# Kernel tuning notes

Hardware: AMD Instinct MI355X
Metric: run time of the kernel (lower is better)

## Reference

```python
import jax, jax.numpy as jnp
import numpy as np

T, DIM, H = 1024, 2048, 16
QLR, KVLR = 1024, 512
NOPE, ROPE, VD = 128, 64, 128
QKD = NOPE + ROPE          # 192
IH, ID, TOPK = 16, 128, 256
EPS = 1e-6

def rmsnorm(x, w):
    return x * jax.lax.rsqrt(jnp.mean(x * x, axis=-1, keepdims=True) + EPS) * w

def layernorm(x, w, b, eps=1e-5):
    m = jnp.mean(x, axis=-1, keepdims=True)
    v = jnp.mean((x - m) ** 2, axis=-1, keepdims=True)
    return (x - m) * jax.lax.rsqrt(v + eps) * w + b

def apply_rope(x, cos, sin):
    # non-interleaved: first half = real, second half = imag
    d = x.shape[-1] // 2
    while cos.ndim < x.ndim:
        cos, sin = cos[:, None], sin[:, None]
    x1, x2 = x[..., :d], x[..., d:]
    return jnp.concatenate([x1 * cos - x2 * sin, x1 * sin + x2 * cos], axis=-1)

def hadamard(x):
    # unnormalized Walsh-Hadamard on last dim (power of 2)
    n = x.shape[-1]
    shape = x.shape
    y, h = x, 1
    while h < n:
        y = y.reshape(shape[:-1] + (-1, 2 * h))
        a, b = y[..., :h], y[..., h:]
        y = jnp.concatenate([a + b, a - b], axis=-1)
        h *= 2
    return y.reshape(shape)

def rotate_activation(x):
    # half-swap then Hadamard on each half
    d = x.shape[-1] // 2
    x1, x2 = x[..., :d], x[..., d:]
    return jnp.concatenate([hadamard(x2), hadamard(x1)], axis=-1)

def setup_inputs() -> dict:
    key = jax.random.key(0)
    ks = jax.random.split(key, 10)
    s = 0.02
    w = lambda k, shp: jax.random.normal(k, shp, jnp.float32) * s
    pos = jnp.arange(T, dtype=jnp.float32)
    inv = 1.0 / (10000.0 ** (jnp.arange(0, ROPE, 2, dtype=jnp.float32) / ROPE))
    ang = pos[:, None] * inv[None, :]
    return {
        'hidden_states': jax.random.normal(ks[0], (T, DIM), jnp.float32),
        'rope_cos': jnp.cos(ang), 'rope_sin': jnp.sin(ang),
        'wq_a': w(ks[1], (QLR, DIM)),
        'q_norm_w': jnp.ones((QLR,), jnp.float32),
        'wq_b': w(ks[2], (H * QKD, QLR)),
        'wkv_a': w(ks[3], (KVLR + ROPE, DIM)),
        'kv_norm_w': jnp.ones((KVLR,), jnp.float32),
        'wkv_b': w(ks[4], (H * (NOPE + VD), KVLR)),
        'wo': w(ks[5], (DIM, H * VD)),
        'iq_norm_w': jnp.ones((QLR,), jnp.float32),
        'iwq_b': w(ks[6], (IH * ID, QLR)),
        'iwk': w(ks[7], (IH * ID, DIM)),
        'k_norm_w': jnp.ones((ID,), jnp.float32),
        'k_norm_b': jnp.zeros((ID,), jnp.float32),
        'wproj': w(ks[8], (IH, DIM)),
    }

def reference(hidden_states, rope_cos, rope_sin, wq_a, q_norm_w, wq_b,
              wkv_a, kv_norm_w, wkv_b, wo, iq_norm_w, iwq_b, iwk,
              k_norm_w, k_norm_b, wproj):
    x = hidden_states
    t = x.shape[0]
    qr = x @ wq_a.T                                   # [t, QLR]

    # ---- lightning indexer: top-k causal token selection ----
    iq = (rmsnorm(qr, iq_norm_w) @ iwq_b.T).reshape(t, IH, ID)
    iq = jnp.concatenate([apply_rope(iq[..., :ROPE], rope_cos, rope_sin), iq[..., ROPE:]], -1)
    iq = rotate_activation(iq)
    ik = layernorm((x @ iwk.T).reshape(t, IH, ID), k_norm_w, k_norm_b)
    ik = jnp.concatenate([apply_rope(ik[..., :ROPE], rope_cos, rope_sin), ik[..., ROPE:]], -1)
    ik = rotate_activation(ik)
    w = (x @ wproj.T) * (IH ** -0.5) * (ID ** -0.5)   # [t, IH]
    dots = jax.nn.relu(jnp.einsum('thd,shd->ths', iq, ik)) * w[:, :, None]
    score = dots.sum(axis=1)                          # [t, t]
    rows = jnp.arange(t)
    score = jnp.where(rows[None, :] <= rows[:, None], score, -jnp.inf)
    _, topk_idx = jax.lax.top_k(score, TOPK)          # [t, TOPK]
    valid = topk_idx <= rows[:, None]
    safe_idx = jnp.where(valid, topk_idx, 0)

    # ---- MLA latent projections ----
    q = (rmsnorm(qr, q_norm_w) @ wq_b.T).reshape(t, H, QKD)
    q_nope, q_pe = q[..., :NOPE], q[..., NOPE:]
    q_pe = apply_rope(q_pe, rope_cos, rope_sin)
    kv_a = x @ wkv_a.T                                # [t, KVLR+ROPE]
    kv = rmsnorm(kv_a[:, :KVLR], kv_norm_w)
    k_pe = apply_rope(kv_a[:, KVLR:], rope_cos, rope_sin)
    wkv = wkv_b.reshape(H, NOPE + VD, KVLR)
    w_k, w_v = wkv[:, :NOPE, :], wkv[:, NOPE:, :]
    q_nope_proj = jnp.einsum('thd,hdc->thc', q_nope, w_k)
    q_key = jnp.concatenate([q_nope_proj, q_pe], -1)  # [t, H, KVLR+ROPE]
    kv_key = jnp.concatenate([kv, k_pe], -1)          # [t, KVLR+ROPE]

    # ---- sparse attention over selected indices ----
    sel = kv_key[safe_idx]                            # [t, TOPK, KVLR+ROPE]
    scale = QKD ** -0.5
    logits = jnp.einsum('thc,tkc->thk', q_key, sel) * scale
    logits = jnp.where(valid[:, None, :], logits, -jnp.inf)
    attn = jax.nn.softmax(logits, axis=-1)
    out_latent = jnp.einsum('thk,tkc->thc', attn, sel[..., :KVLR])
    out_v = jnp.einsum('thc,hdc->thd', out_latent, w_v)
    return out_v.reshape(t, H * VD) @ wo.T            # [t, DIM]
```

## Files before the change

kernel.cpp:

```cpp
#include <hip/hip_runtime.h>
#include <hip/hip_bf16.h>
#include <math.h>

#define T_     1024
#define DIM_   2048
#define H_     16
#define QLR_   1024
#define KVLR_  512
#define NOPE_  128
#define ROPE_  64
#define VD_    128
#define QKD_   192
#define IH_    16
#define ID_    128
#define TOPK_  256
#define CKV_   576

#define SCALE_W    0.022097086912079608f
#define SCALE_LOG  0.07216878364870323f

typedef short bfrag __attribute__((ext_vector_type(8)));
typedef float ffrag __attribute__((ext_vector_type(4)));

__device__ __forceinline__ unsigned short f2bf(float f) {
    union { __hip_bfloat16 h; unsigned short u; } c; c.h = __float2bfloat16(f); return c.u;
}
__device__ __forceinline__ float bf2f(unsigned short u) {
    union { unsigned short u; __hip_bfloat16 h; } c; c.u = u; return __bfloat162float(c.h);
}

struct CastSeg { const float* src; unsigned short* hi; unsigned short* lo; };
struct CastDesc { CastSeg seg[6]; int bstart[7]; int nseg; };

__global__ __launch_bounds__(256) void castm_k(CastDesc d)
{
    int b = blockIdx.x, s = 0;
    #pragma unroll
    for (int i = 1; i < 6; ++i) if (i < d.nseg && b >= d.bstart[i]) s = i;
    long base = ((long)(b - d.bstart[s]) * 256 + threadIdx.x) * 4;
    float4 v = *(const float4*)(d.seg[s].src + base);
    ushort4 h4;
    h4.x = f2bf(v.x); h4.y = f2bf(v.y); h4.z = f2bf(v.z); h4.w = f2bf(v.w);
    *(ushort4*)(d.seg[s].hi + base) = h4;
    if (d.seg[s].lo) {
        ushort4 l4;
        l4.x = f2bf(v.x - bf2f(h4.x));
        l4.y = f2bf(v.y - bf2f(h4.y));
        l4.z = f2bf(v.z - bf2f(h4.z));
        l4.w = f2bf(v.w - bf2f(h4.w));
        *(ushort4*)(d.seg[s].lo + base) = l4;
    }
}

__global__ __launch_bounds__(256) void qrnorm_k(const float* __restrict__ qr,
    const float* __restrict__ iqw, const float* __restrict__ qw,
    unsigned short* __restrict__ qriq_hi, unsigned short* __restrict__ qriq_lo,
    unsigned short* __restrict__ qrq_hi)
{
    int t = blockIdx.x, tid = threadIdx.x;
    long base = (long)t * QLR_ + tid * 4;
    float4 v = *(const float4*)(qr + base);
    __shared__ float red[256];
    red[tid] = v.x * v.x + v.y * v.y + v.z * v.z + v.w * v.w;
    __syncthreads();
    for (int off = 128; off; off >>= 1) { if (tid < off) red[tid] += red[tid + off]; __syncthreads(); }
    float r = rsqrtf(red[0] / (float)QLR_ + 1e-6f);
    int col = tid * 4;
    float4 wi = *(const float4*)(iqw + col);
    float4 wq = *(const float4*)(qw + col);
    float s[4] = {v.x, v.y, v.z, v.w};
    float wiv[4] = {wi.x, wi.y, wi.z, wi.w};
    float wqv[4] = {wq.x, wq.y, wq.z, wq.w};
    ushort4 h4, l4, g4;
    unsigned short* hp = (unsigned short*)&h4;
    unsigned short* lp = (unsigned short*)&l4;
    unsigned short* gp = (unsigned short*)&g4;
    #pragma unroll
    for (int i = 0; i < 4; ++i) {
        float ai = s[i] * wiv[i] * r;
        float aq = s[i] * wqv[i] * r;
        hp[i] = f2bf(ai);
        lp[i] = f2bf(ai - bf2f(hp[i]));
        gp[i] = f2bf(aq);
    }
    *(ushort4*)(qriq_hi + base) = h4;
    *(ushort4*)(qriq_lo + base) = l4;
    *(ushort4*)(qrq_hi + base) = g4;
}

__global__ __launch_bounds__(256) void gemm_bt_mfma_k(
    const unsigned short* __restrict__ A, const unsigned short* __restrict__ B,
    void* __restrict__ Cv, long sA, long sB, long sC,
    int lda, int ldb, int ldc, int N, int K, int obf)
{
    A += (long)blockIdx.z * sA;
    B += (long)blockIdx.z * sB;
    __shared__ unsigned short As[128 * 40];
    __shared__ unsigned short Bs[128 * 40];
    const int tid = threadIdx.x;
    const int bm = blockIdx.y * 128, bn = blockIdx.x * 128;
    const int wave = tid >> 6, lane = tid & 63;
    const int wm = (wave >> 1) * 64, wn = (wave & 1) * 64;
    const int lm = lane & 15, quad = lane >> 4;

    ffrag acc[4][4];
    #pragma unroll
    for (int mi = 0; mi < 4; ++mi)
        #pragma unroll
        for (int ni = 0; ni < 4; ++ni)
            #pragma unroll
            for (int r = 0; r < 4; ++r) acc[mi][ni][r] = 0.f;

    const int srow = tid >> 1, shalf = tid & 1;
    const long aoff = (long)(bm + srow) * lda + shalf * 16;
    int brow = bn + srow; if (brow > N - 1) brow = N - 1;
    const long boff = (long)brow * ldb + shalf * 16;
    unsigned short* la = As + srow * 40 + shalf * 16;
    unsigned short* lb = Bs + srow * 40 + shalf * 16;

    uint4 va0 = *(const uint4*)(A + aoff);
    uint4 va1 = *(const uint4*)(A + aoff + 8);
    uint4 vb0 = *(const uint4*)(B + boff);
    uint4 vb1 = *(const uint4*)(B + boff + 8);

    for (int k0 = 0; k0 < K; k0 += 32) {
        __syncthreads();
        *(uint4*)la = va0; *(uint4*)(la + 8) = va1;
        *(uint4*)lb = vb0; *(uint4*)(lb + 8) = vb1;
        __syncthreads();
        if (k0 + 32 < K) {
            va0 = *(const uint4*)(A + aoff + k0 + 32);
            va1 = *(const uint4*)(A + aoff + k0 + 40);
            vb0 = *(const uint4*)(B + boff + k0 + 32);
            vb1 = *(const uint4*)(B + boff + k0 + 40);
        }
        bfrag af[4], bf[4];
        #pragma unroll
        for (int mi = 0; mi < 4; ++mi)
            af[mi] = *(const bfrag*)(As + (wm + mi * 16 + lm) * 40 + quad * 8);
        #pragma unroll
        for (int ni = 0; ni < 4; ++ni)
            bf[ni] = *(const bfrag*)(Bs + (wn + ni * 16 + lm) * 40 + quad * 8);
        #pragma unroll
        for (int mi = 0; mi < 4; ++mi)
            #pragma unroll
            for (int ni = 0; ni < 4; ++ni)
                acc[mi][ni] = __builtin_amdgcn_mfma_f32_16x16x32_bf16(
                    af[mi], bf[ni], acc[mi][ni], 0, 0, 0);
    }

    #pragma unroll
    for (int mi = 0; mi < 4; ++mi)
        #pragma unroll
        for (int ni = 0; ni < 4; ++ni) {
            int n = bn + wn + ni * 16 + lm;
            if (n < N) {
                int mb = bm + wm + mi * 16 + quad * 4;
                if (obf) {
                    unsigned short* C = (unsigned short*)Cv + (long)blockIdx.z * sC;
                    #pragma unroll
                    for (int r = 0; r < 4; ++r)
                        C[(long)(mb + r) * ldc + n] = f2bf(acc[mi][ni][r]);
                } else {
                    float* C = (float*)Cv + (long)blockIdx.z * sC;
                    #pragma unroll
                    for (int r = 0; r < 4; ++r)
                        C[(long)(mb + r) * ldc + n] = acc[mi][ni][r];
                }
            }
        }
}

struct GSeg {
    const void* A; const void* Al; const void* B; const void* Bl;
    void* C; void* C2;
    long sA, sB, sC;
    int lda, ldb, ldc, N, K, bnx, bmx, mode, obf;
};
struct GDesc { GSeg seg[4]; int bstart[5]; int nseg; };

__global__ __launch_bounds__(256) void mgemm_k(GDesc d)
{
    __shared__ unsigned short Ahs[64 * 72], Als[64 * 72], Bhs[64 * 72], Bls[64 * 72];
    const int tid = threadIdx.x;
    const int b = blockIdx.x;
    int s = 0;
    #pragma unroll
    for (int i = 1; i < 4; ++i) if (i < d.nseg && b >= d.bstart[i]) s = i;
    const int rel = b - d.bstart[s];
    const int mode = d.seg[s].mode;

    if (mode == 2) {
        const float* src = (const float*)d.seg[s].A;
        unsigned short* hi = (unsigned short*)d.seg[s].C;
        unsigned short* lo = (unsigned short*)d.seg[s].C2;
        long base = ((long)rel * 256 + tid) * 4;
        float4 v = *(const float4*)(src + base);
        ushort4 h4;
        h4.x = f2bf(v.x); h4.y = f2bf(v.y); h4.z = f2bf(v.z); h4.w = f2bf(v.w);
        *(ushort4*)(hi + base) = h4;
        if (lo) {
            ushort4 l4;
            l4.x = f2bf(v.x - bf2f(h4.x));
            l4.y = f2bf(v.y - bf2f(h4.y));
            l4.z = f2bf(v.z - bf2f(h4.z));
            l4.w = f2bf(v.w - bf2f(h4.w));
            *(ushort4*)(lo + base) = l4;
        }
        return;
    }
    if (mode == 3) {
        const float* x = (const float*)d.seg[s].A;
        const float* wproj = (const float*)d.seg[s].B;
        float* wt = (float*)d.seg[s].C;
        float* xs = (float*)Ahs;
        int t = rel;
        for (int c = tid; c < DIM_; c += 256) xs[c] = x[(long)t * DIM_ + c];
        __syncthreads();
        int wave = tid >> 6, lane = tid & 63;
        #pragma unroll
        for (int i = 0; i < 4; ++i) {
            int h = wave * 4 + i;
            float sum = 0.f;
            for (int c = lane; c < DIM_; c += 64) sum += xs[c] * wproj[(long)h * DIM_ + c];
            for (int off = 32; off; off >>= 1) sum += __shfl_xor(sum, off, 64);
            if (lane == 0) wt[(long)t * IH_ + h] = sum * SCALE_W;
        }
        return;
    }
    if (mode == 4) {
        const float* in = (const float*)d.seg[s].A;
        unsigned short* out = (unsigned short*)d.seg[s].C;
        int h = rel >> 6, c0 = (rel & 15) * 32, d0 = ((rel >> 4) & 3) * 32;
        float (*tt)[33] = (float(*)[33])(void*)Ahs;
        int tx = tid & 31, ty = tid >> 5;
        #pragma unroll
        for (int i = 0; i < 4; ++i)
            tt[ty + i * 8][tx] = in[(long)(h * 256 + d0 + ty + i * 8) * 512 + c0 + tx];
        __syncthreads();
        #pragma unroll
        for (int i = 0; i < 4; ++i)
            out[((long)h * 512 + c0 + ty + i * 8) * 128 + d0 + tx] = f2bf(tt[tx][ty + i * 8]);
        return;
    }
    if (mode == 5) {
        const float* q = (const float*)d.seg[s].A;
        const float* cosb = (const float*)d.seg[s].B;
        const float* sinb = (const float*)d.seg[s].Bl;
        unsigned short* qk = (unsigned short*)d.seg[s].C;
        int row = rel * 8 + (tid >> 5);
        int i = tid & 31;
        int t = row / H_;
        const float* qp = q + (long)row * QKD_ + NOPE_;
        float x1 = qp[i], x2 = qp[i + 32];
        float c = cosb[t * 32 + i], sn = sinb[t * 32 + i];
        unsigned short* o = qk + (long)row * CKV_ + 512;
        o[i]      = f2bf(x1 * c - x2 * sn);
        o[i + 32] = f2bf(x1 * sn + x2 * c);
        return;
    }

    const GSeg g = d.seg[s];
    const bool three = (mode == 1);
    const int per = g.bnx * g.bmx;
    const int z = rel / per;
    const int r2 = rel - z * per;
    const int bm = (r2 / g.bnx) * 64, bn = (r2 % g.bnx) * 64;
    const unsigned short* A  = (const unsigned short*)g.A + (long)z * g.sA;
    const unsigned short* B  = (const unsigned short*)g.B + (long)z * g.sB;
    const unsigned short* Alp = (const unsigned short*)g.Al;
    const unsigned short* Blp = (const unsigned short*)g.Bl;

    const int wave = tid >> 6, lane = tid & 63;
    const int wm = (wave >> 1) * 32, wn = (wave & 1) * 32;
    const int lm = lane & 15, quad = lane >> 4;

    ffrag acc[2][2];
    #pragma unroll
    for (int mi = 0; mi < 2; ++mi)
        #pragma unroll
        for (int ni = 0; ni < 2; ++ni)
            #pragma unroll
            for (int r = 0; r < 4; ++r) acc[mi][ni][r] = 0.f;

    const int srow = tid >> 2, schunk = tid & 3;
    const long aoff = (long)(bm + srow) * g.lda + schunk * 8;
    int brow = bn + srow; if (brow > g.N - 1) brow = g.N - 1;
    const long boff = (long)brow * g.ldb + schunk * 8;
    const int loff = srow * 72 + schunk * 8;

    uint4 va0, va1, vb0, vb1, wa0, wa1, wb0, wb1;
    va0 = *(const uint4*)(A + aoff);
    va1 = *(const uint4*)(A + aoff + 32);
    vb0 = *(const uint4*)(B + boff);
    vb1 = *(const uint4*)(B + boff + 32);
    if (three) {
        wa0 = *(const uint4*)(Alp + aoff);
        wa1 = *(const uint4*)(Alp + aoff + 32);
        wb0 = *(const uint4*)(Blp + boff);
        wb1 = *(const uint4*)(Blp + boff + 32);
    }

    for (int k0 = 0; k0 < g.K; k0 += 64) {
        __syncthreads();
        *(uint4*)(Ahs + loff) = va0; *(uint4*)(Ahs + loff + 32) = va1;
        *(uint4*)(Bhs + loff) = vb0; *(uint4*)(Bhs + loff + 32) = vb1;
        if (three) {
            *(uint4*)(Als + loff) = wa0; *(uint4*)(Als + loff + 32) = wa1;
            *(uint4*)(Bls + loff) = wb0; *(uint4*)(Bls + loff + 32) = wb1;
        }
        __syncthreads();
        if (k0 + 64 < g.K) {
            va0 = *(const uint4*)(A + aoff + k0 + 64);
            va1 = *(const uint4*)(A + aoff + k0 + 96);
            vb0 = *(const uint4*)(B + boff + k0 + 64);
            vb1 = *(const uint4*)(B + boff + k0 + 96);
            if (three) {
                wa0 = *(const uint4*)(Alp + aoff + k0 + 64);
                wa1 = *(const uint4*)(Alp + aoff + k0 + 96);
                wb0 = *(const uint4*)(Blp + boff + k0 + 64);
                wb1 = *(const uint4*)(Blp + boff + k0 + 96);
            }
        }
        bfrag ah[2][2], bh[2][2], al[2][2], bl[2][2];
        #pragma unroll
        for (int mi = 0; mi < 2; ++mi)
            #pragma unroll
            for (int ks = 0; ks < 2; ++ks)
                ah[mi][ks] = *(const bfrag*)(Ahs + (wm + mi * 16 + lm) * 72 + ks * 32 + quad * 8);
        #pragma unroll
        for (int ni = 0; ni < 2; ++ni)
            #pragma unroll
            for (int ks = 0; ks < 2; ++ks)
                bh[ni][ks] = *(const bfrag*)(Bhs + (wn + ni * 16 + lm) * 72 + ks * 32 + quad * 8);
        if (three) {
            #pragma unroll
            for (int mi = 0; mi < 2; ++mi)
                #pragma unroll
                for (int ks = 0; ks < 2; ++ks)
                    al[mi][ks] = *(const bfrag*)(Als + (wm + mi * 16 + lm) * 72 + ks * 32 + quad * 8);
            #pragma unroll
            for (int ni = 0; ni < 2; ++ni)
                #pragma unroll
                for (int ks = 0; ks < 2; ++ks)
                    bl[ni][ks] = *(const bfrag*)(Bls + (wn + ni * 16 + lm) * 72 + ks * 32 + quad * 8);
        }
        #pragma unroll
        for (int mi = 0; mi < 2; ++mi)
            #pragma unroll
            for (int ni = 0; ni < 2; ++ni) {
                acc[mi][ni] = __builtin_amdgcn_mfma_f32_16x16x32_bf16(ah[mi][0], bh[ni][0], acc[mi][ni], 0, 0, 0);
                if (three) {
                    acc[mi][ni] = __builtin_amdgcn_mfma_f32_16x16x32_bf16(ah[mi][0], bl[ni][0], acc[mi][ni], 0, 0, 0);
                    acc[mi][ni] = __builtin_amdgcn_mfma_f32_16x16x32_bf16(al[mi][0], bh[ni][0], acc[mi][ni], 0, 0, 0);
                }
                acc[mi][ni] = __builtin_amdgcn_mfma_f32_16x16x32_bf16(ah[mi][1], bh[ni][1], acc[mi][ni], 0, 0, 0);
                if (three) {
                    acc[mi][ni] = __builtin_amdgcn_mfma_f32_16x16x32_bf16(ah[mi][1], bl[ni][1], acc[mi][ni], 0, 0, 0);
                    acc[mi][ni] = __builtin_amdgcn_mfma_f32_16x16x32_bf16(al[mi][1], bh[ni][1], acc[mi][ni], 0, 0, 0);
                }
            }
    }

    #pragma unroll
    for (int mi = 0; mi < 2; ++mi)
        #pragma unroll
        for (int ni = 0; ni < 2; ++ni) {
            int n = bn + wn + ni * 16 + lm;
            if (n < g.N) {
                int mb = bm + wm + mi * 16 + quad * 4;
                if (g.obf) {
                    unsigned short* C = (unsigned short*)g.C + (long)z * g.sC;
                    #pragma unroll
                    for (int r = 0; r < 4; ++r)
                        C[(long)(mb + r) * g.ldc + n] = f2bf(acc[mi][ni][r]);
                } else {
                    float* C = (float*)g.C + (long)z * g.sC;
                    #pragma unroll
                    for (int r = 0; r < 4; ++r)
                        C[(long)(mb + r) * g.ldc + n] = acc[mi][ni][r];
                }
            }
        }
}

__global__ __launch_bounds__(256) void mtrans_k(
    const float* __restrict__ iq, unsigned short* __restrict__ iqh, unsigned short* __restrict__ iql,
    const float* __restrict__ ik, unsigned short* __restrict__ ikh, unsigned short* __restrict__ ikl,
    const float* __restrict__ knw, const float* __restrict__ knb,
    const float* __restrict__ kva, unsigned short* __restrict__ kvb, const float* __restrict__ kvnw,
    const float* __restrict__ cosb, const float* __restrict__ sinb)
{
    __shared__ float red[256];
    __shared__ float rsh;
    const int b = blockIdx.x, tid = threadIdx.x;
    if (b < 8192) {
        const bool isq = b < 4096;
        int rb = isq ? b : b - 4096;
        int row = rb * 4 + (tid >> 6);
        int p = tid & 63;
        int t = row >> 4;
        const float* src = isq ? iq : ik;
        float a = src[(long)row * 128 + p];
        float bb = src[(long)row * 128 + 64 + p];
        if (!isq) {
            float ssum = a + bb;
            #pragma unroll
            for (int o = 1; o < 64; o <<= 1) ssum += __shfl_xor(ssum, o, 64);
            float m = ssum * (1.f / 128.f);
            float da = a - m, db = bb - m;
            float v = da * da + db * db;
            #pragma unroll
            for (int o = 1; o < 64; o <<= 1) v += __shfl_xor(v, o, 64);
            float r = rsqrtf(v * (1.f / 128.f) + 1e-5f);
            a = da * r * knw[p] + knb[p];
            bb = db * r * knw[64 + p] + knb[64 + p];
        }
        float c = cosb[t * 32 + (p & 31)], sn = sinb[t * 32 + (p & 31)];
        float asw = __shfl_xor(a, 32, 64);
        a = (p < 32) ? (a * c - asw * sn) : (asw * sn + a * c);
        #pragma unroll
        for (int h = 1; h < 64; h <<= 1) {
            float a2 = __shfl_xor(a, h, 64);
            float b2 = __shfl_xor(bb, h, 64);
            a = (p & h) ? (a2 - a) : (a + a2);
            bb = (p & h) ? (b2 - bb) : (bb + b2);
        }
        unsigned short* hi = isq ? iqh : ikh;
        unsigned short* lo = isq ? iql : ikl;
        unsigned short hb = f2bf(bb), ha = f2bf(a);
        hi[(long)row * 128 + p] = hb;
        hi[(long)row * 128 + 64 + p] = ha;
        lo[(long)row * 128 + p] = f2bf(bb - bf2f(hb));
        lo[(long)row * 128 + 64 + p] = f2bf(a - bf2f(ha));
    } else {
        int t = b - 8192;
        const float* a = kva + (long)t * CKV_;
        unsigned short* o = kvb + (long)t * CKV_;
        float v0 = a[tid], v1 = a[tid + 256];
        red[tid] = v0 * v0 + v1 * v1; __syncthreads();
        for (int off = 128; off; off >>= 1) { if (tid < off) red[tid] += red[tid + off]; __syncthreads(); }
        if (tid == 0) rsh = rsqrtf(red[0] / (float)KVLR_ + 1e-6f);
        __syncthreads();
        float rs = rsh;
        o[tid]       = f2bf(v0 * rs * kvnw[tid]);
        o[tid + 256] = f2bf(v1 * rs * kvnw[tid + 256]);
        if (tid < 32) {
            float x1 = a[512 + tid], x2 = a[544 + tid];
            float c = cosb[t * 32 + tid], sn = sinb[t * 32 + tid];
            o[512 + tid] = f2bf(x1 * c - x2 * sn);
            o[544 + tid] = f2bf(x1 * sn + x2 * c);
        }
    }
}

__global__ __launch_bounds__(256) void score3_k(
    const unsigned short* __restrict__ iqh, const unsigned short* __restrict__ iql,
    const unsigned short* __restrict__ ikh, const unsigned short* __restrict__ ikl,
    const float* __restrict__ wtok, float* __restrict__ scorep)
{
    const int bt = blockIdx.y, bs = blockIdx.x;
    if (bs > bt) return;
    const int hz = blockIdx.z;
    const int h0 = hz * 4;
    float* score = scorep + (long)hz * (T_ * T_);
    __shared__ unsigned short Ah[64 * 72], Al[64 * 72], Bh[64 * 72], Bl[64 * 72];
    __shared__ float wts[64][16];
    const int tid = threadIdx.x;
    const int wave = tid >> 6, lane = tid & 63;
    const int wm = (wave >> 1) * 32, wn = (wave & 1) * 32;
    const int lm = lane & 15, quad = lane >> 4;
    const int t0 = bt * 64, s0 = bs * 64;
    const int srow = tid >> 2, schunk = tid & 3;
    const int loff = srow * 72 + schunk * 8;

    for (int e = tid; e < 1024; e += 256)
        wts[e >> 4][e & 15] = wtok[(long)(t0 + (e >> 4)) * IH_ + (e & 15)];

    const long abase = (long)(t0 + srow) * 2048 + schunk * 8 + h0 * 128;
    const long bbase = (long)(s0 + srow) * 2048 + schunk * 8 + h0 * 128;

    uint4 pah0 = *(const uint4*)(iqh + abase);
    uint4 pah1 = *(const uint4*)(iqh + abase + 32);
    uint4 pal0 = *(const uint4*)(iql + abase);
    uint4 pal1 = *(const uint4*)(iql + abase + 32);
    uint4 pbh0 = *(const uint4*)(ikh + bbase);
    uint4 pbh1 = *(const uint4*)(ikh + bbase + 32);
    uint4 pbl0 = *(const uint4*)(ikl + bbase);
    uint4 pbl1 = *(const uint4*)(ikl + bbase + 32);

    float accf[2][2][4] = {};

    for (int hh = 0; hh < 4; ++hh) {
        const int h = h0 + hh;
        ffrag acch[2][2];
        #pragma unroll
        for (int mi = 0; mi < 2; ++mi)
            #pragma unroll
            for (int ni = 0; ni < 2; ++ni)
                #pragma unroll
                for (int r = 0; r < 4; ++r) acch[mi][ni][r] = 0.f;

        #pragma unroll
        for (int k0 = 0; k0 < ID_; k0 += 64) {
            __syncthreads();
            *(uint4*)(Ah + loff) = pah0; *(uint4*)(Ah + loff + 32) = pah1;
            *(uint4*)(Al + loff) = pal0; *(uint4*)(Al + loff + 32) = pal1;
            *(uint4*)(Bh + loff) = pbh0; *(uint4*)(Bh + loff + 32) = pbh1;
            *(uint4*)(Bl + loff) = pbl0; *(uint4*)(Bl + loff + 32) = pbl1;
            __syncthreads();
            int step = hh * 2 + (k0 >> 6) + 1;
            if (step < 8) {
                long off = (long)(step >> 1) * 128 + (step & 1) * 64;
                pah0 = *(const uint4*)(iqh + abase + off);
                pah1 = *(const uint4*)(iqh + abase + off + 32);
                pal0 = *(const uint4*)(iql + abase + off);
                pal1 = *(const uint4*)(iql + abase + off + 32);
                pbh0 = *(const uint4*)(ikh + bbase + off);
                pbh1 = *(const uint4*)(ikh + bbase + off + 32);
                pbl0 = *(const uint4*)(ikl + bbase + off);
                pbl1 = *(const uint4*)(ikl + bbase + off + 32);
            }
            bfrag ahf[2][2], alf[2][2], bhf[2][2], blf[2][2];
            #pragma unroll
            for (int mi = 0; mi < 2; ++mi)
                #pragma unroll
                for (int ks = 0; ks < 2; ++ks) {
                    ahf[mi][ks] = *(const bfrag*)(Ah + (wm + mi * 16 + lm) * 72 + ks * 32 + quad * 8);
                    alf[mi][ks] = *(const bfrag*)(Al + (wm + mi * 16 + lm) * 72 + ks * 32 + quad * 8);
                }
            #pragma unroll
            for (int ni = 0; ni < 2; ++ni)
                #pragma unroll
                for (int ks = 0; ks < 2; ++ks) {
                    bhf[ni][ks] = *(const bfrag*)(Bh + (wn + ni * 16 + lm) * 72 + ks * 32 + quad * 8);
                    blf[ni][ks] = *(const bfrag*)(Bl + (wn + ni * 16 + lm) * 72 + ks * 32 + quad * 8);
                }
            #pragma unroll
            for (int mi = 0; mi < 2; ++mi)
                #pragma unroll
                for (int ni = 0; ni < 2; ++ni) {
                    acch[mi][ni] = __builtin_amdgcn_mfma_f32_16x16x32_bf16(ahf[mi][0], bhf[ni][0], acch[mi][ni], 0, 0, 0);
                    acch[mi][ni] = __builtin_amdgcn_mfma_f32_16x16x32_bf16(ahf[mi][0], blf[ni][0], acch[mi][ni], 0, 0, 0);
                    acch[mi][ni] = __builtin_amdgcn_mfma_f32_16x16x32_bf16(alf[mi][0], bhf[ni][0], acch[mi][ni], 0, 0, 0);
                    acch[mi][ni] = __builtin_amdgcn_mfma_f32_16x16x32_bf16(ahf[mi][1], bhf[ni][1], acch[mi][ni], 0, 0, 0);
                    acch[mi][ni] = __builtin_amdgcn_mfma_f32_16x16x32_bf16(ahf[mi][1], blf[ni][1], acch[mi][ni], 0, 0, 0);
                    acch[mi][ni] = __builtin_amdgcn_mfma_f32_16x16x32_bf16(alf[mi][1], bhf[ni][1], acch[mi][ni], 0, 0, 0);
                }
        }
        #pragma unroll
        for (int mi = 0; mi < 2; ++mi) {
            float wr[4];
            #pragma unroll
            for (int r = 0; r < 4; ++r) wr[r] = wts[wm + mi * 16 + quad * 4 + r][h];
            #pragma unroll
            for (int ni = 0; ni < 2; ++ni)
                #pragma unroll
                for (int r = 0; r < 4; ++r)
                    accf[mi][ni][r] += fmaxf(acch[mi][ni][r], 0.f) * wr[r];
        }
    }
    #pragma unroll
    for (int mi = 0; mi < 2; ++mi)
        #pragma unroll
        for (int ni = 0; ni < 2; ++ni) {
            int s = s0 + wn + ni * 16 + lm;
            int tb = t0 + wm + mi * 16 + quad * 4;
            #pragma unroll
            for (int r = 0; r < 4; ++r)
                score[(long)(tb + r) * T_ + s] = accf[mi][ni][r];
        }
}

__global__ __launch_bounds__(512) void topk_k(const float* __restrict__ scorep, int* __restrict__ topk)
{
    int t = blockIdx.x, tid = threadIdx.x;
    __shared__ float v[1024];
    __shared__ int ix[1024];
    const float* p0 = scorep + (long)t * T_;
    const float* p1 = p0 + (long)1 * T_ * T_;
    const float* p2 = p0 + (long)2 * T_ * T_;
    const float* p3 = p0 + (long)3 * T_ * T_;
    for (int i = tid; i < 1024; i += 512) {
        v[i] = (i <= t) ? (p0[i] + p1[i] + p2[i] + p3[i]) : -INFINITY;
        ix[i] = i;
    }
    __syncthreads();
    for (int k = 2; k <= 1024; k <<= 1) {
        for (int j = k >> 1; j > 0; j >>= 1) {
            for (int i = tid; i < 1024; i += 512) {
                int l = i ^ j;
                if (l > i) {
                    bool up = ((i & k) == 0);
                    float vi = v[i], vl = v[l];
                    int xi = ix[i], xl = ix[l];
                    bool iBetter = (vi > vl) || (vi == vl && xi < xl);
                    bool doSwap = up ? !iBetter : iBetter;
                    if (doSwap) { v[i] = vl; v[l] = vi; ix[i] = xl; ix[l] = xi; }
                }
            }
            __syncthreads();
        }
    }
    if (tid < 256) topk[(long)t * TOPK_ + tid] = ix[tid];
}

__global__ __launch_bounds__(256, 4) void attn3_k(
    const unsigned short* __restrict__ qkeyb, const unsigned short* __restrict__ kvb,
    const int* __restrict__ topkp, unsigned short* __restrict__ olat)
{
    __shared__ __align__(16) unsigned short U[13568];
    __shared__ float red[16 * 17];
    __shared__ int kidx[256];
    unsigned short* Qbf = U;
    float*          Lg  = (float*)U;
    unsigned short* VT0 = U;
    unsigned short* VT1 = U + 4608;
    unsigned short* Pbf = U + 9344;

    const int t = blockIdx.x, tid = threadIdx.x;
    const int wave = tid >> 6, lane = tid & 63;
    const int lm = lane & 15, quad = lane >> 4;

    kidx[tid] = topkp[(long)t * TOPK_ + tid];
    const uint2* q2 = (const uint2*)(qkeyb + (long)t * (H_ * CKV_));
    #pragma unroll
    for (int rep = 0; rep < 9; ++rep) {
        int e = rep * 256 + tid;
        uint2 v = q2[e];
        int f = e * 4, h = f / CKV_, c = f - h * CKV_;
        *(uint2*)(Qbf + h * 584 + c) = v;
    }
    int myk0 = topkp[(long)t * TOPK_ + wave * 64 + 0 * 16 + lm];
    int myk1 = topkp[(long)t * TOPK_ + wave * 64 + 1 * 16 + lm];
    int myk2 = topkp[(long)t * TOPK_ + wave * 64 + 2 * 16 + lm];
    int myk3 = topkp[(long)t * TOPK_ + wave * 64 + 3 * 16 + lm];
    __syncthreads();

    ffrag acc[4];
    #pragma unroll
    for (int ni = 0; ni < 4; ++ni)
        #pragma unroll
        for (int r = 0; r < 4; ++r) acc[ni][r] = 0.f;

    const unsigned short* kb0 = kvb + (long)myk0 * CKV_ + quad * 8;
    const unsigned short* kb1 = kvb + (long)myk1 * CKV_ + quad * 8;
    const unsigned short* kb2 = kvb + (long)myk2 * CKV_ + quad * 8;
    const unsigned short* kb3 = kvb + (long)myk3 * CKV_ + quad * 8;

    bfrag ba[4], bb[4], bc[4];
    #define LDT(DST, C) { \
        DST[0] = *(const bfrag*)(kb0 + (C)); \
        DST[1] = *(const bfrag*)(kb1 + (C)); \
        DST[2] = *(const bfrag*)(kb2 + (C)); \
        DST[3] = *(const bfrag*)(kb3 + (C)); }
    #define PHA_STEP(I, BUF) { \
        bfrag af = *(const bfrag*)(Qbf + lm * 584 + (I) * 32 + quad * 8); \
        _Pragma("unroll") \
        for (int ni = 0; ni < 4; ++ni) \
            acc[ni] = __builtin_amdgcn_mfma_f32_16x16x32_bf16(af, BUF[ni], acc[ni], 0, 0, 0); \
        if ((I) < 15) LDT(BUF, (I) * 32 + 96) }

    LDT(ba, 0) LDT(bb, 32) LDT(bc, 64)
    PHA_STEP(0, ba)  PHA_STEP(1, bb)  PHA_STEP(2, bc)
    PHA_STEP(3, ba)  PHA_STEP(4, bb)  PHA_STEP(5, bc)
    PHA_STEP(6, ba)  PHA_STEP(7, bb)  PHA_STEP(8, bc)
    PHA_STEP(9, ba)  PHA_STEP(10, bb) PHA_STEP(11, bc)
    PHA_STEP(12, ba) PHA_STEP(13, bb) PHA_STEP(14, bc)
    PHA_STEP(15, ba) PHA_STEP(16, bb) PHA_STEP(17, bc)
    #undef PHA_STEP
    #undef LDT

    __syncthreads();
    #pragma unroll
    for (int ni = 0; ni < 4; ++ni)
        #pragma unroll
        for (int r = 0; r < 4; ++r)
            Lg[(quad * 4 + r) * 260 + wave * 64 + ni * 16 + lm] = acc[ni][r];
    __syncthreads();

    {
        int h = tid >> 4, j = tid & 15;
        float m = -INFINITY;
        #pragma unroll
        for (int kk = 0; kk < 16; ++kk) {
            int key = j * 16 + kk;
            if (kidx[key] <= t) m = fmaxf(m, Lg[h * 260 + key]);
        }
        red[h * 17 + j] = m;
        __syncthreads();
        float mh = -INFINITY;
        #pragma unroll
        for (int jj = 0; jj < 16; ++jj) mh = fmaxf(mh, red[h * 17 + jj]);
        __syncthreads();
        float s = 0.f;
        float pv[16];
        #pragma unroll
        for (int kk = 0; kk < 16; ++kk) {
            int key = j * 16 + kk;
            float e = (kidx[key] <= t) ? expf(Lg[h * 260 + key] * SCALE_LOG - mh * SCALE_LOG) : 0.f;
            pv[kk] = e; s += e;
        }
        red[h * 17 + j] = s;
        __syncthreads();
        float sh = 0.f;
        #pragma unroll
        for (int jj = 0; jj < 16; ++jj) sh += red[h * 17 + jj];
        float inv = 1.f / sh;
        #pragma unroll
        for (int kk = 0; kk < 16; ++kk)
            Pbf[h * 264 + j * 16 + kk] = f2bf(pv[kk] * inv);
    }

    const int kpair = tid & 15, cgrp = tid >> 4;
    ffrag acc2[2];
    #pragma unroll
    for (int ci = 0; ci < 2; ++ci)
        #pragma unroll
        for (int r = 0; r < 4; ++r) acc2[ci][r] = 0.f;

    uint4 ga0, gb0, ga1, gb1;
    #define PREFB(GA, GB, IT) { \
        int ka_ = kidx[((IT) & 7) * 32 + 2 * kpair]; \
        int kb_ = kidx[((IT) & 7) * 32 + 2 * kpair + 1]; \
        long co_ = (long)(((IT) >> 3) * 128 + cgrp * 8); \
        GA = *(const uint4*)(kvb + (long)ka_ * CKV_ + co_); \
        GB = *(const uint4*)(kvb + (long)kb_ * CKV_ + co_); }
    #define STOREB(GA, GB, BUF) { \
        const unsigned short* pa_ = (const unsigned short*)&GA; \
        const unsigned short* pb_ = (const unsigned short*)&GB; \
        _Pragma("unroll") \
        for (int i_ = 0; i_ < 8; ++i_) \
            *(unsigned int*)((BUF) + (cgrp * 8 + i_) * 36 + 2 * kpair) = \
                (unsigned int)pa_[i_] | ((unsigned int)pb_[i_] << 16); }
    #define MFMAB(BUF, IT) { \
        bfrag pa = *(const bfrag*)(Pbf + lm * 264 + ((IT) & 7) * 32 + quad * 8); \
        _Pragma("unroll") \
        for (int ci = 0; ci < 2; ++ci) { \
            int c = wave * 32 + ci * 16 + lm; \
            bfrag bv; \
            ((uint2*)&bv)[0] = *(const uint2*)((BUF) + c * 36 + quad * 8); \
            ((uint2*)&bv)[1] = *(const uint2*)((BUF) + c * 36 + quad * 8 + 4); \
            acc2[ci] = __builtin_amdgcn_mfma_f32_16x16x32_bf16(pa, bv, acc2[ci], 0, 0, 0); } }
    #define OLATST(IT) { \
        int p_ = (IT) >> 3; \
        _Pragma("unroll") \
        for (int ci = 0; ci < 2; ++ci) \
            _Pragma("unroll") \
            for (int r = 0; r < 4; ++r) \
                olat[((long)t * H_ + quad * 4 + r) * 512 + p_ * 128 + wave * 32 + ci * 16 + lm] \
                    = f2bf(acc2[ci][r]); \
        _Pragma("unroll") \
        for (int ci = 0; ci < 2; ++ci) \
            _Pragma("unroll") \
            for (int r = 0; r < 4; ++r) acc2[ci][r] = 0.f; }
    #define LGKBAR() { asm volatile("s_waitcnt lgkmcnt(0)" ::: "memory"); \
                       __builtin_amdgcn_s_barrier(); }

    PREFB(ga0, gb0, 0);
    PREFB(ga1, gb1, 1);
    LGKBAR();
    STOREB(ga0, gb0, VT0);
    LGKBAR();
    for (int it = 0; it < 32; it += 2) {
        STOREB(ga1, gb1, VT1);
        MFMAB(VT0, it);
        if (it + 2 < 32) PREFB(ga0, gb0, it + 2);
        LGKBAR();
        if (it + 2 < 32) STOREB(ga0, gb0, VT0);
        MFMAB(VT1, it + 1);
        if (it + 3 < 32) PREFB(ga1, gb1, it + 3);
        if (((it + 1) & 7) == 7) OLATST(it + 1);
        LGKBAR();
    }
    #undef PREFB
    #undef STOREB
    #undef MFMAB
    #undef OLATST
    #undef LGKBAR
}

extern "C" void kernel_launch(void* const* d_in, const int* in_sizes, int n_in,
                              void* d_out, int out_size, void* d_ws, size_t ws_size,
                              hipStream_t stream)
{
    const float* x          = (const float*)d_in[0];
    const float* cosb       = (const float*)d_in[1];
    const float* sinb       = (const float*)d_in[2];
    const float* wq_a       = (const float*)d_in[3];
    const float* q_norm_w   = (const float*)d_in[4];
    const float* wq_b       = (const float*)d_in[5];
    const float* wkv_a      = (const float*)d_in[6];
    const float* kv_norm_w  = (const float*)d_in[7];
    const float* wkv_b      = (const float*)d_in[8];
    const float* wo         = (const float*)d_in[9];
    const float* iq_norm_w  = (const float*)d_in[10];
    const float* iwq_b      = (const float*)d_in[11];
    const float* iwk        = (const float*)d_in[12];
    const float* k_norm_w   = (const float*)d_in[13];
    const float* k_norm_b   = (const float*)d_in[14];
    const float* wproj      = (const float*)d_in[15];
    float* out = (float*)d_out;

    float* ws    = (float*)d_ws;
    float* qr    = ws;
    float* wtok  = ws + 1049600;
    int*   topk  = (int*)(ws + 1655808);
    float* qkey  = ws + 1917952;
    float* outv  = ws + 11355136;
    float* U0    = ws + 13452288;
    float* iq    = U0;
    float* ik    = U0 + 2097152;
    float* kva   = U0 + 4194304;
    float* qbuf  = U0 + 4784128;
    float* scorep = U0;

    unsigned short* qkey_u = (unsigned short*)qkey;
    unsigned short* wqa_hi  = qkey_u;
    unsigned short* wqa_lo  = qkey_u + 2097152;
    unsigned short* iwk_hi  = qkey_u + 4194304;
    unsigned short* iwk_lo  = qkey_u + 8388608;
    unsigned short* iwqb_hi = qkey_u + 12582912;
    unsigned short* iwqb_lo = qkey_u + 14680064;
    unsigned short* qriq_hi = qkey_u + 16777216;
    unsigned short* qriq_lo = qkey_u + 17825792;
    unsigned short* iqbf_hi = qkey_u;
    unsigned short* iqbf_lo = qkey_u + 2097152;
    unsigned short* ikbf_hi = qkey_u + 4194304;
    unsigned short* ikbf_lo = qkey_u + 6291456;
    unsigned short* qkey_bf = qkey_u;
    unsigned short* wkvb_bf = qkey_u + 9437184;
    unsigned short* wo_bf   = qkey_u;
    unsigned short* q_u     = (unsigned short*)qbuf;
    unsigned short* x_hi    = q_u;
    unsigned short* x_lo    = q_u + 2097152;
    unsigned short* wkva_hi = q_u + 4194304;
    unsigned short* outv_u  = (unsigned short*)outv;
    unsigned short* wqb_hi  = outv_u;
    unsigned short* qrq_hi  = outv_u + 3145728;
    unsigned short* outv_bf = outv_u;
    unsigned short* qbf     = (unsigned short*)iq;
    unsigned short* wkT     = (unsigned short*)ik;
    unsigned short* kvb     = (unsigned short*)qr;
    unsigned short* olat_bf = (unsigned short*)U0;

    {
        CastDesc d;
        d.seg[0] = { x,      x_hi,    x_lo    };
        d.seg[1] = { wq_a,   wqa_hi,  wqa_lo  };
        d.seg[2] = { iwk,    iwk_hi,  iwk_lo  };
        d.seg[3] = { iwq_b,  iwqb_hi, iwqb_lo };
        d.seg[4] = { wkv_a,  wkva_hi, nullptr };
        d.seg[5] = { wq_b,   wqb_hi,  nullptr };
        d.bstart[0] = 0;     d.bstart[1] = 2048;  d.bstart[2] = 4096;
        d.bstart[3] = 8192;  d.bstart[4] = 10240; d.bstart[5] = 11392;
        d.bstart[6] = 14464; d.nseg = 6;
        castm_k<<<14464, 256, 0, stream>>>(d);
    }

    {
        GDesc d{};
        d.nseg = 3;
        d.bstart[0] = 0; d.bstart[1] = 256; d.bstart[2] = 768; d.bstart[3] = 1792;
        GSeg& s0 = d.seg[0];
        s0.A = x_hi; s0.Al = x_lo; s0.B = wqa_hi; s0.Bl = wqa_lo; s0.C = qr;
        s0.lda = DIM_; s0.ldb = DIM_; s0.ldc = QLR_; s0.N = QLR_; s0.K = DIM_;
        s0.bnx = 16; s0.bmx = 16; s0.mode = 1; s0.obf = 0;
        GSeg& s1 = d.seg[1];
        s1.A = x_hi; s1.Al = x_lo; s1.B = iwk_hi; s1.Bl = iwk_lo; s1.C = ik;
        s1.lda = DIM_; s1.ldb = DIM_; s1.ldc = IH_ * ID_; s1.N = IH_ * ID_; s1.K = DIM_;
        s1.bnx = 32; s1.bmx = 16; s1.mode = 1; s1.obf = 0;
        GSeg& s2 = d.seg[2];
        s2.A = x; s2.B = wproj; s2.C = wtok; s2.mode = 3;
        mgemm_k<<<1792, 256, 0, stream>>>(d);
    }

    qrnorm_k<<<T_, 256, 0, stream>>>(qr, iq_norm_w, q_norm_w, qriq_hi, qriq_lo, qrq_hi);

    {
        GDesc d{};
        d.nseg = 3;
        d.bstart[0] = 0; d.bstart[1] = 512; d.bstart[2] = 656; d.bstart[3] = 2704;
        GSeg& s0 = d.seg[0];
        s0.A = qriq_hi; s0.Al = qriq_lo; s0.B = iwqb_hi; s0.Bl = iwqb_lo; s0.C = iq;
        s0.lda = QLR_; s0.ldb = QLR_; s0.ldc = IH_ * ID_; s0.N = IH_ * ID_; s0.K = QLR_;
        s0.bnx = 32; s0.bmx = 16; s0.mode = 1; s0.obf = 0;
        GSeg& s1 = d.seg[1];
        s1.A = x_hi; s1.B = wkva_hi; s1.C = kva;
        s1.lda = DIM_; s1.ldb = DIM_; s1.ldc = CKV_; s1.N = CKV_; s1.K = DIM_;
        s1.bnx = 9; s1.bmx = 16; s1.mode = 0; s1.obf = 0;
        GSeg& s2 = d.seg[2];
        s2.A = wkv_b; s2.C = wkvb_bf; s2.C2 = nullptr; s2.mode = 2;
        mgemm_k<<<2704, 256, 0, stream>>>(d);
    }

    {
        GDesc d{};
        d.nseg = 1;
        d.bstart[0] = 0; d.bstart[1] = 768;
        GSeg& s0 = d.seg[0];
        s0.A = qrq_hi; s0.B = wqb_hi; s0.C = qbuf;
        s0.lda = QLR_; s0.ldb = QLR_; s0.ldc = H_ * QKD_; s0.N = H_ * QKD_; s0.K = QLR_;
        s0.bnx = 48; s0.bmx = 16; s0.mode = 0; s0.obf = 0;
        mgemm_k<<<768, 256, 0, stream>>>(d);
    }

    mtrans_k<<<9216, 256, 0, stream>>>(iq, iqbf_hi, iqbf_lo, ik, ikbf_hi, ikbf_lo,
                                       k_norm_w, k_norm_b, kva, kvb, kv_norm_w, cosb, sinb);

    score3_k<<<dim3(T_/64, T_/64, 4), 256, 0, stream>>>(iqbf_hi, iqbf_lo, ikbf_hi, ikbf_lo, wtok, scorep);
    topk_k<<<T_, 512, 0, stream>>>(scorep, topk);

    {
        GDesc d{};
        d.nseg = 3;
        d.bstart[0] = 0; d.bstart[1] = 3072; d.bstart[2] = 4096; d.bstart[3] = 6144;
        GSeg& s0 = d.seg[0];
        s0.A = qbuf; s0.C = qbf; s0.C2 = nullptr; s0.mode = 2;
        GSeg& s1 = d.seg[1];
        s1.A = wkv_b; s1.C = wkT; s1.mode = 4;
        GSeg& s2 = d.seg[2];
        s2.A = qbuf; s2.B = cosb; s2.Bl = sinb; s2.C = qkey_bf; s2.mode = 5;
        mgemm_k<<<6144, 256, 0, stream>>>(d);
    }

    gemm_bt_mfma_k<<<dim3(KVLR_/128, T_/128, H_), 256, 0, stream>>>(
        qbf, wkT, qkey_bf, 192L, 65536L, 576L, H_*QKD_, ID_, H_*CKV_, KVLR_, ID_, 1);

    attn3_k<<<T_, 256, 0, stream>>>(qkey_bf, kvb, topk, olat_bf);

    {
        GDesc d{};
        d.nseg = 2;
        d.bstart[0] = 0; d.bstart[1] = 512; d.bstart[2] = 4608;
        GSeg& s0 = d.seg[0];
        s0.A = olat_bf; s0.B = wkvb_bf + (long)NOPE_ * KVLR_; s0.C = outv_bf;
        s0.sA = 512; s0.sB = (long)(NOPE_ + VD_) * KVLR_; s0.sC = VD_;
        s0.lda = H_ * KVLR_; s0.ldb = KVLR_; s0.ldc = H_ * VD_; s0.N = VD_; s0.K = KVLR_;
        s0.bnx = 2; s0.bmx = 16; s0.mode = 0; s0.obf = 1;
        GSeg& s1 = d.seg[1];
        s1.A = wo; s1.C = wo_bf; s1.C2 = nullptr; s1.mode = 2;
        mgemm_k<<<4608, 256, 0, stream>>>(d);
    }

    {
        GDesc d{};
        d.nseg = 1;
        d.bstart[0] = 0; d.bstart[1] = 512;
        GSeg& s0 = d.seg[0];
        s0.A = outv_bf; s0.B = wo_bf; s0.C = out;
        s0.lda = H_ * VD_; s0.ldb = H_ * VD_; s0.ldc = DIM_; s0.N = DIM_; s0.K = H_ * VD_;
        s0.bnx = 32; s0.bmx = 16; s0.mode = 0; s0.obf = 0;
        mgemm_k<<<512, 256, 0, stream>>>(d);
    }

    (void)in_sizes; (void)n_in; (void)out_size; (void)ws_size;
}
```

Before: 493.4 us.

## Merge transform kernel into wq_b GEMM launch and move wo cast into attention

Folds the separate indexer-transform and kv-norm kernel into the wq_b GEMM launch as new segment modes 6 and 7. The standalone wo bf16 cast moves from the output-projection launch into extra blocks of the attention kernel, and two scratch buffers swap locations to allow this. The aim is fewer kernel launches and letting independent small work fill idle compute units next to the GEMM and attention. In exchange, the fused kernels carry more code and shared memory, which could lower occupancy. Co-scheduling also now depends on the buffers not aliasing.

Result: no change. 500.5 us (+1.4%).

```diff
diff --git a/kernel.cpp b/kernel.cpp
--- a/kernel.cpp
+++ b/kernel.cpp
@@ -259,6 +259,75 @@
         o[i + 32] = f2bf(x1 * sn + x2 * c);
         return;
     }
+    if (mode == 6) {
+        const float* src = (const float*)d.seg[s].A;
+        unsigned short* hi = (unsigned short*)d.seg[s].C;
+        unsigned short* lo = (unsigned short*)d.seg[s].C2;
+        const float* cosb = (const float*)d.seg[s].B;
+        const float* sinb = (const float*)d.seg[s].Bl;
+        const float* knw  = (const float*)d.seg[s].Al;
+        const float* knb  = (const float*)(void*)d.seg[s].sA;
+        int row = rel * 4 + (tid >> 6);
+        int p = tid & 63;
+        int t = row >> 4;
+        float a = src[(long)row * 128 + p];
+        float bb = src[(long)row * 128 + 64 + p];
+        if (knw) {
+            float ssum = a + bb;
+            #pragma unroll
+            for (int o = 1; o < 64; o <<= 1) ssum += __shfl_xor(ssum, o, 64);
+            float m = ssum * (1.f / 128.f);
+            float da = a - m, db = bb - m;
+            float v = da * da + db * db;
+            #pragma unroll
+            for (int o = 1; o < 64; o <<= 1) v += __shfl_xor(v, o, 64);
+            float r = rsqrtf(v * (1.f / 128.f) + 1e-5f);
+            a = da * r * knw[p] + knb[p];
+            bb = db * r * knw[64 + p] + knb[64 + p];
+        }
+        float c = cosb[t * 32 + (p & 31)], sn = sinb[t * 32 + (p & 31)];
+        float asw = __shfl_xor(a, 32, 64);
+        a = (p < 32) ? (a * c - asw * sn) : (asw * sn + a * c);
+        #pragma unroll
+        for (int h = 1; h < 64; h <<= 1) {
+            float a2 = __shfl_xor(a, h, 64);
+            float b2 = __shfl_xor(bb, h, 64);
+            a = (p & h) ? (a2 - a) : (a + a2);
+            bb = (p & h) ? (b2 - bb) : (bb + b2);
+        }
+        unsigned short hb = f2bf(bb), ha = f2bf(a);
+        hi[(long)row * 128 + p] = hb;
+        hi[(long)row * 128 + 64 + p] = ha;
+        lo[(long)row * 128 + p] = f2bf(bb - bf2f(hb));
+        lo[(long)row * 128 + 64 + p] = f2bf(a - bf2f(ha));
+        return;
+    }
+    if (mode == 7) {
+        const float* kva = (const float*)d.seg[s].A;
+        unsigned short* kvb = (unsigned short*)d.seg[s].C;
+        const float* kvnw = (const float*)d.seg[s].B;
+        const float* cosb = (const float*)d.seg[s].Bl;
+        const float* sinb = (const float*)d.seg[s].Al;
+        float* red = (float*)Ahs;
+        int t = rel;
+        const float* a = kva + (long)t * CKV_;
+        unsigned short* o = kvb + (long)t * CKV_;
+        float v0 = a[tid], v1 = a[tid + 256];
+        red[tid] = v0 * v0 + v1 * v1; __syncthreads();
+        for (int off = 128; off; off >>= 1) { if (tid < off) red[tid] += red[tid + off]; __syncthreads(); }
+        if (tid == 0) red[256] = rsqrtf(red[0] / (float)KVLR_ + 1e-6f);
+        __syncthreads();
+        float rs = red[256];
+        o[tid]       = f2bf(v0 * rs * kvnw[tid]);
+        o[tid + 256] = f2bf(v1 * rs * kvnw[tid + 256]);
+        if (tid < 32) {
+            float x1 = a[512 + tid], x2 = a[544 + tid];
+            float c = cosb[t * 32 + tid], sn = sinb[t * 32 + tid];
+            o[512 + tid] = f2bf(x1 * c - x2 * sn);
+            o[544 + tid] = f2bf(x1 * sn + x2 * c);
+        }
+        return;
+    }
 
     const GSeg g = d.seg[s];
     const bool three = (mode == 1);
@@ -382,76 +451,6 @@
                 }
             }
         }
-}
-
-__global__ __launch_bounds__(256) void mtrans_k(
-    const float* __restrict__ iq, unsigned short* __restrict__ iqh, unsigned short* __restrict__ iql,
-    const float* __restrict__ ik, unsigned short* __restrict__ ikh, unsigned short* __restrict__ ikl,
-    const float* __restrict__ knw, const float* __restrict__ knb,
-    const float* __restrict__ kva, unsigned short* __restrict__ kvb, const float* __restrict__ kvnw,
-    const float* __restrict__ cosb, const float* __restrict__ sinb)
-{
-    __shared__ float red[256];
-    __shared__ float rsh;
-    const int b = blockIdx.x, tid = threadIdx.x;
-    if (b < 8192) {
-        const bool isq = b < 4096;
-        int rb = isq ? b : b - 4096;
-        int row = rb * 4 + (tid >> 6);
-        int p = tid & 63;
-        int t = row >> 4;
-        const float* src = isq ? iq : ik;
-        float a = src[(long)row * 128 + p];
-        float bb = src[(long)row * 128 + 64 + p];
-        if (!isq) {
-            float ssum = a + bb;
-            #pragma unroll
-            for (int o = 1; o < 64; o <<= 1) ssum += __shfl_xor(ssum, o, 64);
-            float m = ssum * (1.f / 128.f);
-            float da = a - m, db = bb - m;
-            float v = da * da + db * db;
-            #pragma unroll
-            for (int o = 1; o < 64; o <<= 1) v += __shfl_xor(v, o, 64);
-            float r = rsqrtf(v * (1.f / 128.f) + 1e-5f);
-            a = da * r * knw[p] + knb[p];
-            bb = db * r * knw[64 + p] + knb[64 + p];
-        }
-        float c = cosb[t * 32 + (p & 31)], sn = sinb[t * 32 + (p & 31)];
-        float asw = __shfl_xor(a, 32, 64);
-        a = (p < 32) ? (a * c - asw * sn) : (asw * sn + a * c);
-        #pragma unroll
-        for (int h = 1; h < 64; h <<= 1) {
-            float a2 = __shfl_xor(a, h, 64);
-            float b2 = __shfl_xor(bb, h, 64);
-            a = (p & h) ? (a2 - a) : (a + a2);
-            bb = (p & h) ? (b2 - bb) : (bb + b2);
-        }
-        unsigned short* hi = isq ? iqh : ikh;
-        unsigned short* lo = isq ? iql : ikl;
-        unsigned short hb = f2bf(bb), ha = f2bf(a);
-        hi[(long)row * 128 + p] = hb;
-        hi[(long)row * 128 + 64 + p] = ha;
-        lo[(long)row * 128 + p] = f2bf(bb - bf2f(hb));
-        lo[(long)row * 128 + 64 + p] = f2bf(a - bf2f(ha));
-    } else {
-        int t = b - 8192;
-        const float* a = kva + (long)t * CKV_;
-        unsigned short* o = kvb + (long)t * CKV_;
-        float v0 = a[tid], v1 = a[tid + 256];
-        red[tid] = v0 * v0 + v1 * v1; __syncthreads();
-        for (int off = 128; off; off >>= 1) { if (tid < off) red[tid] += red[tid + off]; __syncthreads(); }
-        if (tid == 0) rsh = rsqrtf(red[0] / (float)KVLR_ + 1e-6f);
-        __syncthreads();
-        float rs = rsh;
-        o[tid]       = f2bf(v0 * rs * kvnw[tid]);
-        o[tid + 256] = f2bf(v1 * rs * kvnw[tid + 256]);
-        if (tid < 32) {
-            float x1 = a[512 + tid], x2 = a[544 + tid];
-            float c = cosb[t * 32 + tid], sn = sinb[t * 32 + tid];
-            o[512 + tid] = f2bf(x1 * c - x2 * sn);
-            o[544 + tid] = f2bf(x1 * sn + x2 * c);
-        }
-    }
 }
 
 __global__ __launch_bounds__(256) void score3_k(
@@ -607,11 +606,23 @@
 
 __global__ __launch_bounds__(256, 4) void attn3_k(
     const unsigned short* __restrict__ qkeyb, const unsigned short* __restrict__ kvb,
-    const int* __restrict__ topkp, unsigned short* __restrict__ olat)
+    const int* __restrict__ topkp, unsigned short* __restrict__ olat,
+    const float* __restrict__ wo, unsigned short* __restrict__ wo_bf)
 {
     __shared__ __align__(16) unsigned short U[13568];
     __shared__ float red[16 * 17];
     __shared__ int kidx[256];
+
+    if (blockIdx.x >= 1024) {
+        int rel = blockIdx.x - 1024;
+        long base = ((long)rel * 256 + threadIdx.x) * 4;
+        float4 v = *(const float4*)(wo + base);
+        ushort4 h4;
+        h4.x = f2bf(v.x); h4.y = f2bf(v.y); h4.z = f2bf(v.z); h4.w = f2bf(v.w);
+        *(ushort4*)(wo_bf + base) = h4;
+        return;
+    }
+
     unsigned short* Qbf = U;
     float*          Lg  = (float*)U;
     unsigned short* VT0 = U;
@@ -830,7 +841,7 @@
     unsigned short* ikbf_lo = qkey_u + 6291456;
     unsigned short* qkey_bf = qkey_u;
     unsigned short* wkvb_bf = qkey_u + 9437184;
-    unsigned short* wo_bf   = qkey_u;
+    unsigned short* outv_bf = qkey_u;
     unsigned short* q_u     = (unsigned short*)qbuf;
     unsigned short* x_hi    = q_u;
     unsigned short* x_lo    = q_u + 2097152;
@@ -838,7 +849,7 @@
     unsigned short* outv_u  = (unsigned short*)outv;
     unsigned short* wqb_hi  = outv_u;
     unsigned short* qrq_hi  = outv_u + 3145728;
-    unsigned short* outv_bf = outv_u;
+    unsigned short* wo_bf   = outv_u;
     unsigned short* qbf     = (unsigned short*)iq;
     unsigned short* wkT     = (unsigned short*)ik;
     unsigned short* kvb     = (unsigned short*)qr;
@@ -896,17 +907,26 @@
 
     {
         GDesc d{};
-        d.nseg = 1;
-        d.bstart[0] = 0; d.bstart[1] = 768;
+        d.nseg = 4;
+        d.bstart[0] = 0; d.bstart[1] = 768; d.bstart[2] = 4864; d.bstart[3] = 8960;
+        d.bstart[4] = 9984;
         GSeg& s0 = d.seg[0];
         s0.A = qrq_hi; s0.B = wqb_hi; s0.C = qbuf;
         s0.lda = QLR_; s0.ldb = QLR_; s0.ldc = H_ * QKD_; s0.N = H_ * QKD_; s0.K = QLR_;
         s0.bnx = 48; s0.bmx = 16; s0.mode = 0; s0.obf = 0;
-        mgemm_k<<<768, 256, 0, stream>>>(d);
-    }
-
-    mtrans_k<<<9216, 256, 0, stream>>>(iq, iqbf_hi, iqbf_lo, ik, ikbf_hi, ikbf_lo,
-                                       k_norm_w, k_norm_b, kva, kvb, kv_norm_w, cosb, sinb);
+        GSeg& s1 = d.seg[1];
+        s1.A = iq; s1.C = iqbf_hi; s1.C2 = iqbf_lo;
+        s1.B = cosb; s1.Bl = sinb; s1.Al = nullptr; s1.sA = 0;
+        s1.mode = 6;
+        GSeg& s2 = d.seg[2];
+        s2.A = ik; s2.C = ikbf_hi; s2.C2 = ikbf_lo;
+        s2.B = cosb; s2.Bl = sinb; s2.Al = k_norm_w; s2.sA = (long)(size_t)k_norm_b;
+        s2.mode = 6;
+        GSeg& s3 = d.seg[3];
+        s3.A = kva; s3.C = kvb; s3.B = kv_norm_w; s3.Bl = cosb; s3.Al = sinb;
+        s3.mode = 7;
+        mgemm_k<<<9984, 256, 0, stream>>>(d);
+    }
 
     score3_k<<<dim3(T_/64, T_/64, 4), 256, 0, stream>>>(iqbf_hi, iqbf_lo, ikbf_hi, ikbf_lo, wtok, scorep);
     topk_k<<<T_, 512, 0, stream>>>(scorep, topk);
@@ -927,20 +947,18 @@
     gemm_bt_mfma_k<<<dim3(KVLR_/128, T_/128, H_), 256, 0, stream>>>(
         qbf, wkT, qkey_bf, 192L, 65536L, 576L, H_*QKD_, ID_, H_*CKV_, KVLR_, ID_, 1);
 
-    attn3_k<<<T_, 256, 0, stream>>>(qkey_bf, kvb, topk, olat_bf);
+    attn3_k<<<1024 + 4096, 256, 0, stream>>>(qkey_bf, kvb, topk, olat_bf, wo, wo_bf);
 
     {
         GDesc d{};
-        d.nseg = 2;
-        d.bstart[0] = 0; d.bstart[1] = 512; d.bstart[2] = 4608;
+        d.nseg = 1;
+        d.bstart[0] = 0; d.bstart[1] = 512;
         GSeg& s0 = d.seg[0];
         s0.A = olat_bf; s0.B = wkvb_bf + (long)NOPE_ * KVLR_; s0.C = outv_bf;
         s0.sA = 512; s0.sB = (long)(NOPE_ + VD_) * KVLR_; s0.sC = VD_;
         s0.lda = H_ * KVLR_; s0.ldb = KVLR_; s0.ldc = H_ * VD_; s0.N = VD_; s0.K = KVLR_;
         s0.bnx = 2; s0.bmx = 16; s0.mode = 0; s0.obf = 1;
-        GSeg& s1 = d.seg[1];
-        s1.A = wo; s1.C = wo_bf; s1.C2 = nullptr; s1.mode = 2;
-        mgemm_k<<<4608, 256, 0, stream>>>(d);
+        mgemm_k<<<512, 256, 0, stream>>>(d);
     }
 
     {
```
